# Kernel tuning notes

Hardware: AMD Instinct MI355X
Metric: run time of the kernel (lower is better)

Reference implementation:

```python
import jax, jax.numpy as jnp
import numpy as np

B, N, C, OUT = 4, 512, 128, 128

def setup_inputs() -> dict:
    key = jax.random.key(0)
    k1, k2, k3 = jax.random.split(key, 3)
    adj_matrix = jax.random.bernoulli(k1, 0.1, (B, N, N)).astype(jnp.float32)
    features = jax.random.normal(k2, (B, N, C), dtype=jnp.float32)
    # xavier_uniform for Linear(2C -> OUT): weight stored here as [2C, OUT]
    limit = float(np.sqrt(6.0 / (2 * C + OUT)))
    W = jax.random.uniform(k3, (2 * C, OUT), minval=-limit, maxval=limit, dtype=jnp.float32)
    b = jnp.zeros((OUT,), dtype=jnp.float32)
    return {"adj_matrix": adj_matrix, "features": features, "W": W, "b": b}

def reference(adj_matrix, features, W, b):
    # pooling aggregator: masked max over neighbors (materializes [B,N,N,C], as in source)
    neg_inf = jnp.finfo(features.dtype).min
    mask = (adj_matrix > 0)[..., None]                      # [B,N,N,1]
    feat_nb = jnp.where(mask, features[:, None, :, :], neg_inf)  # [B,N,N,C]
    agg = jnp.max(feat_nb, axis=2)                          # [B,N,C]
    agg = jnp.where(jnp.isfinite(agg), agg, 0.0)
    neigh = jax.nn.relu(agg)
    combined = jnp.concatenate([features, neigh], axis=-1)  # [B,N,2C]
    return jnp.einsum('bnc,co->bno', combined, W) + b       # [B,N,OUT]
```

## Files before the change

kernel.cpp:

```cpp
#include <hip/hip_runtime.h>
#include <hip/hip_bf16.h>
#include <float.h>


#define Bsz 4
#define Nn  512
#define Cc  128
#define OUTn 128
#define NNODES (Bsz * Nn)
#define KK (2 * Cc)
#define ROWP 264

typedef __bf16 bf16x8 __attribute__((ext_vector_type(8)));
typedef float  f32x4  __attribute__((ext_vector_type(4)));

static __device__ __forceinline__ unsigned short f2bf(float x) {
    __hip_bfloat16 h = __float2bfloat16(x);
    return *reinterpret_cast<unsigned short*>(&h);
}
static __device__ __forceinline__ __bf16 f2bf16(float x) {
    unsigned short u = f2bf(x);
    return *reinterpret_cast<__bf16*>(&u);
}

__global__ __launch_bounds__(1024) void sage_fused(
    const float* __restrict__ adj,
    const float* __restrict__ feat,
    const float* __restrict__ W,
    const float* __restrict__ bias,
    float* __restrict__ out)
{
    const int bid = blockIdx.x;
    const int mt  = bid >> 1;
    const int rh  = bid & 1;
    const int w = threadIdx.x >> 6;
    const int l = threadIdx.x & 63;

    __shared__ unsigned short nbr[16][256];
    __shared__ float2 pm[16][64];
    __shared__ unsigned short sA[16][ROWP];

    const int slot = w & 7;
    const int half = w >> 3;
    const int node = mt * 16 + rh * 8 + slot;
    const int b = node >> 9;
    const int i = node & (Nn - 1);

    const float* adjrow = adj + (size_t)node * Nn;
    const float2* f2 = (const float2*)(feat + (size_t)b * Nn * Cc);

    int cnt = 0;
    #pragma unroll
    for (int ch = 0; ch < 4; ++ch) {
        int j = half * 256 + ch * 64 + l;
        float a = adjrow[j];
        unsigned long long mask = __ballot(a > 0.0f);
        int pos = __popcll(mask & ((1ull << l) - 1ull));
        if (a > 0.0f) nbr[w][cnt + pos] = (unsigned short)j;
        cnt += __popcll(mask);
    }
    if (cnt > 0) {
        unsigned short p0 = nbr[w][0];
        int padded = (cnt + 7) & ~7;
        if (l < padded - cnt) nbr[w][cnt + l] = p0;
        cnt = padded;
    }

    float m0 = -FLT_MAX, m1 = -FLT_MAX;
    for (int k = 0; k < cnt; k += 8) {
        int j0 = nbr[w][k + 0], j1 = nbr[w][k + 1];
        int j2 = nbr[w][k + 2], j3 = nbr[w][k + 3];
        int j4 = nbr[w][k + 4], j5 = nbr[w][k + 5];
        int j6 = nbr[w][k + 6], j7 = nbr[w][k + 7];
        float2 v0 = f2[j0 * 64 + l];
        float2 v1 = f2[j1 * 64 + l];
        float2 v2 = f2[j2 * 64 + l];
        float2 v3 = f2[j3 * 64 + l];
        float2 v4 = f2[j4 * 64 + l];
        float2 v5 = f2[j5 * 64 + l];
        float2 v6 = f2[j6 * 64 + l];
        float2 v7 = f2[j7 * 64 + l];
        m0 = fmaxf(m0, fmaxf(fmaxf(fmaxf(v0.x, v1.x), fmaxf(v2.x, v3.x)),
                             fmaxf(fmaxf(v4.x, v5.x), fmaxf(v6.x, v7.x))));
        m1 = fmaxf(m1, fmaxf(fmaxf(fmaxf(v0.y, v1.y), fmaxf(v2.y, v3.y)),
                             fmaxf(fmaxf(v4.y, v5.y), fmaxf(v6.y, v7.y))));
    }
    pm[w][l] = make_float2(m0, m1);

    {
        unsigned int* z = (unsigned int*)&sA[8][0];
        for (int idx = threadIdx.x; idx < 8 * (ROWP / 2); idx += 1024) z[idx] = 0u;
    }
    __syncthreads();

    if (w < 8) {
        float2 a0 = pm[w][l], a1 = pm[w + 8][l];
        float n0 = fmaxf(fmaxf(a0.x, a1.x), 0.0f);
        float n1 = fmaxf(fmaxf(a0.y, a1.y), 0.0f);
        float2 s = f2[i * 64 + l];

        ushort2* crow = (ushort2*)&sA[w][0];
        ushort2 sv; sv.x = f2bf(s.x); sv.y = f2bf(s.y);
        ushort2 nv; nv.x = f2bf(n0);  nv.y = f2bf(n1);
        crow[l]      = sv;
        crow[64 + l] = nv;
    }
    __syncthreads();

    if (w < 8) {
        const int nt = w;
        const int frow = l & 15;
        const int koff = (l >> 4) * 8;
        const float* wp = W + nt * 16 + frow;

        f32x4 acc = {0.f, 0.f, 0.f, 0.f};
        #pragma unroll
        for (int ks = 0; ks < KK / 32; ++ks) {
            bf16x8 af = *(const bf16x8*)&sA[frow][ks * 32 + koff];
            bf16x8 bfr;
            #pragma unroll
            for (int j = 0; j < 8; ++j) {
                bfr[j] = f2bf16(wp[(size_t)(ks * 32 + koff + j) * OUTn]);
            }
            acc = __builtin_amdgcn_mfma_f32_16x16x32_bf16(af, bfr, acc, 0, 0, 0);
        }

        const int col = l & 15;
        const int r0  = (l >> 4) * 4;
        const float bv = bias[nt * 16 + col];
        #pragma unroll
        for (int r = 0; r < 4; ++r) {
            int row = r0 + r;
            if (row < 8) {
                out[(size_t)(mt * 16 + rh * 8 + row) * OUTn + nt * 16 + col]
                    = acc[r] + bv;
            }
        }
    }
}

extern "C" void kernel_launch(void* const* d_in, const int* in_sizes, int n_in,
                              void* d_out, int out_size, void* d_ws, size_t ws_size,
                              hipStream_t stream) {
    const float* adj  = (const float*)d_in[0];
    const float* feat = (const float*)d_in[1];
    const float* W    = (const float*)d_in[2];
    const float* bias = (const float*)d_in[3];
    float* out = (float*)d_out;

    sage_fused<<<dim3(NNODES / 8), dim3(1024), 0, stream>>>(
        adj, feat, W, bias, out);
}
```

Measured before the change: 67.13 us.

## Process four nodes per block with quarter-row splits and split-K MFMA

Each block now handles 4 nodes instead of 8, with four waves per node each scanning a quarter of the adjacency row via float2 loads. The launch doubles the block count to spread the work over more CUs. The GEMM stage splits K across all 16 waves and reduces partial sums through shared memory, so no waves sit idle. Neighbor indices are read as packed uint4 vectors. In exchange, the W loads and MFMA work per output row roughly double, since the 16-row MFMA tile now holds only 4 valid rows.

```diff
diff --git a/kernel.cpp b/kernel.cpp
--- a/kernel.cpp
+++ b/kernel.cpp
@@ -23,7 +23,7 @@
     return *reinterpret_cast<__bf16*>(&u);
 }
 
-__global__ __launch_bounds__(1024) void sage_fused(
+__global__ __launch_bounds__(1024, 8) void sage_fused(
     const float* __restrict__ adj,
     const float* __restrict__ feat,
     const float* __restrict__ W,
@@ -31,33 +31,34 @@
     float* __restrict__ out)
 {
     const int bid = blockIdx.x;
-    const int mt  = bid >> 1;
-    const int rh  = bid & 1;
     const int w = threadIdx.x >> 6;
     const int l = threadIdx.x & 63;
 
-    __shared__ unsigned short nbr[16][256];
+    const int slot = w & 3;
+    const int q    = w >> 2;
+    const int node = bid * 4 + slot;
+    const int b = node >> 9;
+    const int i = node & (Nn - 1);
+
+    __shared__ unsigned short nbr[16][128];
     __shared__ float2 pm[16][64];
     __shared__ unsigned short sA[16][ROWP];
-
-    const int slot = w & 7;
-    const int half = w >> 3;
-    const int node = mt * 16 + rh * 8 + slot;
-    const int b = node >> 9;
-    const int i = node & (Nn - 1);
+    __shared__ f32x4 accbuf[8][16];
 
     const float* adjrow = adj + (size_t)node * Nn;
     const float2* f2 = (const float2*)(feat + (size_t)b * Nn * Cc);
 
     int cnt = 0;
-    #pragma unroll
-    for (int ch = 0; ch < 4; ++ch) {
-        int j = half * 256 + ch * 64 + l;
-        float a = adjrow[j];
-        unsigned long long mask = __ballot(a > 0.0f);
-        int pos = __popcll(mask & ((1ull << l) - 1ull));
-        if (a > 0.0f) nbr[w][cnt + pos] = (unsigned short)j;
-        cnt += __popcll(mask);
+    {
+        float2 a = *(const float2*)(adjrow + q * 128 + 2 * l);
+        unsigned long long mk = __ballot(a.x > 0.0f);
+        int pos = __popcll(mk & ((1ull << l) - 1ull));
+        if (a.x > 0.0f) nbr[w][pos] = (unsigned short)(q * 128 + 2 * l);
+        cnt = __popcll(mk);
+        mk = __ballot(a.y > 0.0f);
+        pos = __popcll(mk & ((1ull << l) - 1ull));
+        if (a.y > 0.0f) nbr[w][cnt + pos] = (unsigned short)(q * 128 + 2 * l + 1);
+        cnt += __popcll(mk);
     }
     if (cnt > 0) {
         unsigned short p0 = nbr[w][0];
@@ -67,11 +68,13 @@
     }
 
     float m0 = -FLT_MAX, m1 = -FLT_MAX;
+    const uint4* nv = (const uint4*)&nbr[w][0];
     for (int k = 0; k < cnt; k += 8) {
-        int j0 = nbr[w][k + 0], j1 = nbr[w][k + 1];
-        int j2 = nbr[w][k + 2], j3 = nbr[w][k + 3];
-        int j4 = nbr[w][k + 4], j5 = nbr[w][k + 5];
-        int j6 = nbr[w][k + 6], j7 = nbr[w][k + 7];
+        uint4 p = nv[k >> 3];
+        int j0 = p.x & 0xffff, j1 = p.x >> 16;
+        int j2 = p.y & 0xffff, j3 = p.y >> 16;
+        int j4 = p.z & 0xffff, j5 = p.z >> 16;
+        int j6 = p.w & 0xffff, j7 = p.w >> 16;
         float2 v0 = f2[j0 * 64 + l];
         float2 v1 = f2[j1 * 64 + l];
         float2 v2 = f2[j2 * 64 + l];
@@ -86,55 +89,53 @@
                              fmaxf(fmaxf(v4.y, v5.y), fmaxf(v6.y, v7.y))));
     }
     pm[w][l] = make_float2(m0, m1);
-
-    {
-        unsigned int* z = (unsigned int*)&sA[8][0];
-        for (int idx = threadIdx.x; idx < 8 * (ROWP / 2); idx += 1024) z[idx] = 0u;
-    }
     __syncthreads();
 
-    if (w < 8) {
-        float2 a0 = pm[w][l], a1 = pm[w + 8][l];
-        float n0 = fmaxf(fmaxf(a0.x, a1.x), 0.0f);
-        float n1 = fmaxf(fmaxf(a0.y, a1.y), 0.0f);
+    if (w < 4) {
+        float2 a0 = pm[w][l],     a1 = pm[w + 4][l];
+        float2 a2 = pm[w + 8][l], a3 = pm[w + 12][l];
+        float n0 = fmaxf(fmaxf(fmaxf(a0.x, a1.x), fmaxf(a2.x, a3.x)), 0.0f);
+        float n1 = fmaxf(fmaxf(fmaxf(a0.y, a1.y), fmaxf(a2.y, a3.y)), 0.0f);
         float2 s = f2[i * 64 + l];
 
         ushort2* crow = (ushort2*)&sA[w][0];
         ushort2 sv; sv.x = f2bf(s.x); sv.y = f2bf(s.y);
-        ushort2 nv; nv.x = f2bf(n0);  nv.y = f2bf(n1);
+        ushort2 nn; nn.x = f2bf(n0);  nn.y = f2bf(n1);
         crow[l]      = sv;
-        crow[64 + l] = nv;
+        crow[64 + l] = nn;
     }
     __syncthreads();
 
-    if (w < 8) {
-        const int nt = w;
-        const int frow = l & 15;
-        const int koff = (l >> 4) * 8;
-        const float* wp = W + nt * 16 + frow;
+    const int nt = w & 7;
+    const int kh = w >> 3;
+    const int frow = l & 15;
+    const int koff = (l >> 4) * 8;
+    const float* wp = W + nt * 16 + frow;
 
-        f32x4 acc = {0.f, 0.f, 0.f, 0.f};
+    f32x4 acc = {0.f, 0.f, 0.f, 0.f};
+    #pragma unroll
+    for (int ks = 0; ks < 4; ++ks) {
+        const int kbase = kh * 128 + ks * 32 + koff;
+        bf16x8 af = *(const bf16x8*)&sA[frow][kbase];
+        bf16x8 bfr;
         #pragma unroll
-        for (int ks = 0; ks < KK / 32; ++ks) {
-            bf16x8 af = *(const bf16x8*)&sA[frow][ks * 32 + koff];
-            bf16x8 bfr;
-            #pragma unroll
-            for (int j = 0; j < 8; ++j) {
-                bfr[j] = f2bf16(wp[(size_t)(ks * 32 + koff + j) * OUTn]);
-            }
-            acc = __builtin_amdgcn_mfma_f32_16x16x32_bf16(af, bfr, acc, 0, 0, 0);
+        for (int j = 0; j < 8; ++j) {
+            bfr[j] = f2bf16(wp[(size_t)(kbase + j) * OUTn]);
         }
+        acc = __builtin_amdgcn_mfma_f32_16x16x32_bf16(af, bfr, acc, 0, 0, 0);
+    }
 
-        const int col = l & 15;
-        const int r0  = (l >> 4) * 4;
+    if (w >= 8 && l < 16) accbuf[nt][l] = acc;
+    __syncthreads();
+
+    if (w < 8 && l < 16) {
+        f32x4 oth = accbuf[nt][l];
+        const int col = l;
         const float bv = bias[nt * 16 + col];
         #pragma unroll
         for (int r = 0; r < 4; ++r) {
-            int row = r0 + r;
-            if (row < 8) {
-                out[(size_t)(mt * 16 + rh * 8 + row) * OUTn + nt * 16 + col]
-                    = acc[r] + bv;
-            }
+            out[(size_t)(bid * 4 + r) * OUTn + nt * 16 + col]
+                = acc[r] + oth[r] + bv;
         }
     }
 }
@@ -148,6 +149,6 @@
     const float* bias = (const float*)d_in[3];
     float* out = (float*)d_out;
 
-    sage_fused<<<dim3(NNODES / 8), dim3(1024), 0, stream>>>(
+    sage_fused<<<dim3(NNODES / 4), dim3(1024), 0, stream>>>(
         adj, feat, W, bias, out);
 }
```

Result: no change. 67.88 us (+1.1%).
